# Kernel tuning notes

Hardware: AMD Instinct MI355X
Metric: run time of the kernel (lower is better)

Reference implementation:

```python
import jax, jax.numpy as jnp
import numpy as np

N_HEAD = 16
HEAD_DIM = 64
ROPE_BASE = 10000.0


def _rope_cos_sin(T, dim, dtype):
    inv_freq = 1.0 / (ROPE_BASE ** (np.arange(0, dim, 2, dtype=np.float32) / dim))
    t = np.arange(T, dtype=np.float32)
    freqs = np.outer(t, inv_freq)              # [T, dim/2]
    emb = np.concatenate([freqs, freqs], -1)   # [T, dim]
    return jnp.asarray(np.cos(emb), dtype), jnp.asarray(np.sin(emb), dtype)


def _rotate_half(x):
    x1, x2 = x[..., : x.shape[-1] // 2], x[..., x.shape[-1] // 2 :]
    return jnp.concatenate([-x2, x1], axis=-1)


def setup_inputs() -> dict:
    key = jax.random.key(0)
    k1, k2, k3 = jax.random.split(key, 3)
    B, T, C = 4, 2048, 1024
    x = jax.random.normal(k1, (B, T, C), jnp.float32)
    w_qkv = jax.random.normal(k2, (C, 3 * C), jnp.float32) * (C ** -0.5)
    w_proj = jax.random.normal(k3, (C, C), jnp.float32) * (C ** -0.5)
    return {"x": x, "w_qkv": w_qkv, "w_proj": w_proj}


def reference(x, w_qkv, w_proj):
    B, T, C = x.shape
    H, D = N_HEAD, HEAD_DIM
    qkv = x @ w_qkv                                   # [B, T, 3C]
    q, k, v = jnp.split(qkv, 3, axis=-1)
    # [B, H, T, D]
    q = q.reshape(B, T, H, D).transpose(0, 2, 1, 3)
    k = k.reshape(B, T, H, D).transpose(0, 2, 1, 3)
    v = v.reshape(B, T, H, D).transpose(0, 2, 1, 3)
    cos, sin = _rope_cos_sin(T, D, x.dtype)           # [T, D]
    q = q * cos + _rotate_half(q) * sin
    k = k * cos + _rotate_half(k) * sin
    scale = D ** -0.5
    scores = jnp.einsum("bhqd,bhkd->bhqk", q, k) * scale
    causal = jnp.tril(jnp.ones((T, T), bool))
    scores = jnp.where(causal, scores, jnp.finfo(scores.dtype).min)
    attn = jax.nn.softmax(scores, axis=-1)
    y = jnp.einsum("bhqk,bhkd->bhqd", attn, v)        # [B, H, T, D]
    y = y.transpose(0, 2, 1, 3).reshape(B, T, C)
    return y @ w_proj
```

## Files before the change

kernel.cpp:

```cpp
#include <hip/hip_runtime.h>
#include <cstdint>

typedef unsigned short u16;
typedef __attribute__((ext_vector_type(4))) float f32x4;
typedef __attribute__((ext_vector_type(4))) unsigned short u16x4;
typedef __attribute__((ext_vector_type(8))) unsigned short u16x8;
typedef __attribute__((ext_vector_type(8))) __bf16 bf16x8;

#define DEV __device__ __forceinline__

DEV u16 f2bf(float f) {
  union { float f; uint32_t u; } x{f};
  uint32_t r = (x.u + 0x7fffu + ((x.u >> 16) & 1u)) >> 16;
  return (u16)r;
}

DEV void gl_lds16(const void* g, void* l) {
  __builtin_amdgcn_global_load_lds((__attribute__((address_space(1))) void*)(g),
                                   (__attribute__((address_space(3))) void*)(l),
                                   16, 0, 0);
}

__global__ __launch_bounds__(256) void cast_f2b(const float* __restrict__ in,
                                                u16* __restrict__ out) {
  int i = blockIdx.x * 256 + threadIdx.x;
  float4 v = ((const float4*)in)[i];
  u16x4 o = { f2bf(v.x), f2bf(v.y), f2bf(v.z), f2bf(v.w) };
  ((u16x4*)out)[i] = o;
}

__global__ __launch_bounds__(256) void transpose_cast(const float* __restrict__ in,
                                                      u16* __restrict__ out, int R, int C) {
  __shared__ float tile[64][65];
  const int c0 = blockIdx.x * 64, r0 = blockIdx.y * 64;
  const int tx = threadIdx.x & 63, ty = threadIdx.x >> 6;
  for (int r = ty; r < 64; r += 4) tile[r][tx] = in[(size_t)(r0 + r) * C + c0 + tx];
  __syncthreads();
  for (int r = ty; r < 64; r += 4) out[(size_t)(c0 + r) * R + r0 + tx] = f2bf(tile[tx][r]);
}

template <int EPI>
__global__ __launch_bounds__(256) void gemm_bt(const u16* __restrict__ A,
                                               const u16* __restrict__ Bt,
                                               u16* __restrict__ qo, u16* __restrict__ ko,
                                               u16* __restrict__ vo, float* __restrict__ outf) {
  extern __shared__ char lds_occupancy_pad[];
  const int K = 1024;
  __shared__ __align__(16) u16 As[128 * 64];
  __shared__ __align__(16) u16 Bs[128 * 64];
  const int m0 = blockIdx.y * 128, n0 = blockIdx.x * 128;
  const int tid = threadIdx.x;
  const int w = tid >> 6, lane = tid & 63, quad = lane >> 4, l15 = lane & 15;
  const int mw = (w >> 1) * 64, nw = (w & 1) * 64;

  const int srow = tid >> 3;
  const int schunk = ((tid & 7) ^ (srow & 7)) * 8;

  f32x4 acc[4][4];
#pragma unroll
  for (int i = 0; i < 4; ++i)
#pragma unroll
    for (int j = 0; j < 4; ++j) acc[i][j] = f32x4{0.f, 0.f, 0.f, 0.f};

  const u16* ga0 = A + (size_t)(m0 + srow) * K + schunk;
  const u16* gb0 = Bt + (size_t)(n0 + srow) * K + schunk;

  const int sw7 = l15 & 7;
  int aoff[4], boff[4];
#pragma unroll
  for (int i = 0; i < 4; ++i) aoff[i] = (mw + i * 16 + l15) * 64;
#pragma unroll
  for (int j = 0; j < 4; ++j) boff[j] = (nw + j * 16 + l15) * 64;
  int coff[2];
#pragma unroll
  for (int kk = 0; kk < 2; ++kk) coff[kk] = ((kk * 4 + quad) ^ sw7) * 8;

  for (int k0 = 0; k0 < K; k0 += 64) {
#pragma unroll
    for (int ss = 0; ss < 4; ++ss) {
      gl_lds16(ga0 + (size_t)ss * 32 * K + k0, As + ss * 2048 + tid * 8);
      gl_lds16(gb0 + (size_t)ss * 32 * K + k0, Bs + ss * 2048 + tid * 8);
    }
    __syncthreads();
#pragma unroll
    for (int kk = 0; kk < 2; ++kk) {
      bf16x8 af[4], bfv[4];
#pragma unroll
      for (int i = 0; i < 4; ++i) af[i] = *(const bf16x8*)(As + aoff[i] + coff[kk]);
#pragma unroll
      for (int j = 0; j < 4; ++j) bfv[j] = *(const bf16x8*)(Bs + boff[j] + coff[kk]);
#pragma unroll
      for (int i = 0; i < 4; ++i)
#pragma unroll
        for (int j = 0; j < 4; ++j)
          acc[i][j] = __builtin_amdgcn_mfma_f32_16x16x32_bf16(af[i], bfv[j], acc[i][j], 0, 0, 0);
    }
    __syncthreads();
  }

  if (EPI == 1) {
#pragma unroll
    for (int i = 0; i < 4; ++i)
#pragma unroll
      for (int j = 0; j < 4; ++j)
#pragma unroll
        for (int r = 0; r < 4; ++r) {
          int row = m0 + mw + i * 16 + quad * 4 + r;
          int col = n0 + nw + j * 16 + l15;
          outf[(size_t)row * 1024 + col] = acc[i][j][r];
        }
    return;
  }
  const int s = n0 >> 10;
  const int hh = ((n0 & 1023) + nw) >> 6;
  if (s == 2) {
#pragma unroll
    for (int i = 0; i < 4; ++i)
#pragma unroll
      for (int r = 0; r < 4; ++r) {
        int row = m0 + mw + i * 16 + quad * 4 + r;
        int b = row >> 11, t = row & 2047;
        size_t base = ((size_t)(b * 16 + hh) * 2048 + t) * 64;
#pragma unroll
        for (int j = 0; j < 4; ++j) vo[base + j * 16 + l15] = f2bf(acc[i][j][r]);
      }
  } else {
    u16* dst = (s == 0) ? qo : ko;
    const float QS = (s == 0) ? 0.18033688011112042f : 1.0f;
    const float C1 = -0.4152410118609203f;
    const float R2PI = 0.15915494309189535f;
    const float inv0 = __builtin_amdgcn_exp2f((float)l15 * C1) * R2PI;
    const float inv1 = __builtin_amdgcn_exp2f((float)(16 + l15) * C1) * R2PI;
#pragma unroll
    for (int i = 0; i < 4; ++i)
#pragma unroll
      for (int r = 0; r < 4; ++r) {
        int row = m0 + mw + i * 16 + quad * 4 + r;
        int b = row >> 11, t = row & 2047;
        size_t base = ((size_t)(b * 16 + hh) * 2048 + t) * 64;
        float tf = (float)t;
        float a0 = tf * inv0; a0 -= floorf(a0);
        float a1 = tf * inv1; a1 -= floorf(a1);
        float c0 = __builtin_amdgcn_cosf(a0), s0 = __builtin_amdgcn_sinf(a0);
        float c1 = __builtin_amdgcn_cosf(a1), s1 = __builtin_amdgcn_sinf(a1);
        float x0 = acc[i][0][r], y0 = acc[i][2][r];
        float x1 = acc[i][1][r], y1 = acc[i][3][r];
        dst[base + l15]      = f2bf((x0 * c0 - y0 * s0) * QS);
        dst[base + 32 + l15] = f2bf((y0 * c0 + x0 * s0) * QS);
        dst[base + 16 + l15] = f2bf((x1 * c1 - y1 * s1) * QS);
        dst[base + 48 + l15] = f2bf((y1 * c1 + x1 * s1) * QS);
      }
  }
}

__global__ __launch_bounds__(256) void transpose_v(const u16* __restrict__ v,
                                                   u16* __restrict__ vt) {
  const int bh = blockIdx.y, t0 = blockIdx.x * 64;
  __shared__ __align__(16) u16 tile[64][72];
  const int tid = threadIdx.x;
  const int row = tid >> 3, col = (tid & 7) * 8;
#pragma unroll
  for (int rr = 0; rr < 2; ++rr) {
    int r = row + rr * 32;
    *(u16x8*)(&tile[r][col]) = *(const u16x8*)(v + ((size_t)bh * 2048 + t0 + r) * 64 + col);
  }
  __syncthreads();
#pragma unroll
  for (int rr = 0; rr < 2; ++rr) {
    int d = row + rr * 32;
    u16x8 o;
#pragma unroll
    for (int j = 0; j < 8; ++j) o[j] = tile[col + j][d];
    *(u16x8*)(vt + ((size_t)bh * 64 + d) * 2048 + t0 + col) = o;
  }
}

__global__ __launch_bounds__(256) void attn_kernel(const u16* __restrict__ q,
                                                   const u16* __restrict__ k,
                                                   const u16* __restrict__ vt,
                                                   u16* __restrict__ y) {
  const int T = 2048;
  const int bh = blockIdx.x;
  const int qi = 15 - blockIdx.y;
  const int q0 = qi * 128;
  const int tid = threadIdx.x;
  const int w = tid >> 6, lane = tid & 63, quad = lane >> 4, l15 = lane & 15;
  __shared__ __align__(16) u16 Ks[64 * 64];
  __shared__ __align__(16) u16 Vs[64 * 64];
  __shared__ __align__(16) u16 Pq[4 * 32 * 72];
  u16* Pw = Pq + w * 32 * 72;

  const int sw = l15 & 7;
  int koff[4][2], voff[4][2];
#pragma unroll
  for (int kf = 0; kf < 4; ++kf) {
    koff[kf][0] = (kf * 16 + l15) * 64 + ((quad ^ sw) * 8);
    koff[kf][1] = (kf * 16 + l15) * 64 + (((quad + 4) ^ sw) * 8);
  }
#pragma unroll
  for (int df = 0; df < 4; ++df) {
    voff[df][0] = (df * 16 + l15) * 64 + ((quad ^ sw) * 8);
    voff[df][1] = (df * 16 + l15) * 64 + (((quad + 4) ^ sw) * 8);
  }
  const int pwoff = l15 * 72 + quad * 4;
  const int proff = l15 * 72 + quad * 8;

  const int r_ = tid >> 3, c_ = tid & 7, ssw = r_ & 7;
  const u16* kg = k + (size_t)bh * T * 64;
  const u16* vg = vt + (size_t)bh * 64 * T;
  const int sk0 = r_ * 64 + (c_ ^ ssw) * 8;
  const int sk1 = (r_ + 32) * 64 + (c_ ^ ssw) * 8;
  const int sv0 = r_ * T + (c_ ^ ssw) * 8;
  const int sv1 = (r_ + 32) * T + (c_ ^ ssw) * 8;

  const int b_ = bh >> 4, h_ = bh & 15;
  const int q0w = q0 + w * 32;

  bf16x8 qf_[2][2];
#pragma unroll
  for (int qf = 0; qf < 2; ++qf)
#pragma unroll
    for (int h = 0; h < 2; ++h)
      qf_[qf][h] = *(const bf16x8*)(q + ((size_t)bh * T + q0w + qf * 16 + l15) * 64 + h * 32 + quad * 8);

  f32x4 o[2][4];
  float li[2] = {0.f, 0.f};
#pragma unroll
  for (int qf = 0; qf < 2; ++qf)
#pragma unroll
    for (int df = 0; df < 4; ++df) o[qf][df] = f32x4{0.f, 0.f, 0.f, 0.f};

  const int nit = 2 * qi + 2;

  for (int it = 0; it < nit; ++it) {
    const int kb = it * 64;
    gl_lds16(kg + (size_t)kb * 64 + sk0, Ks + tid * 8);
    gl_lds16(kg + (size_t)kb * 64 + sk1, Ks + 2048 + tid * 8);
    gl_lds16(vg + kb + sv0, Vs + tid * 8);
    gl_lds16(vg + kb + sv1, Vs + 2048 + tid * 8);
    __syncthreads();

    bf16x8 ka[4][2];
#pragma unroll
    for (int kf = 0; kf < 4; ++kf) {
      ka[kf][0] = *(const bf16x8*)(Ks + koff[kf][0]);
      ka[kf][1] = *(const bf16x8*)(Ks + koff[kf][1]);
    }
    f32x4 st[2][4];
#pragma unroll
    for (int kf = 0; kf < 4; ++kf)
#pragma unroll
      for (int qf = 0; qf < 2; ++qf) {
        f32x4 s = f32x4{0.f, 0.f, 0.f, 0.f};
        s = __builtin_amdgcn_mfma_f32_16x16x32_bf16(ka[kf][0], qf_[qf][0], s, 0, 0, 0);
        s = __builtin_amdgcn_mfma_f32_16x16x32_bf16(ka[kf][1], qf_[qf][1], s, 0, 0, 0);
        st[qf][kf] = s;
      }

    if (it >= nit - 2) {
#pragma unroll
      for (int qf = 0; qf < 2; ++qf) {
        const int qrow = q0w + qf * 16 + l15;
#pragma unroll
        for (int kf = 0; kf < 4; ++kf)
#pragma unroll
          for (int r = 0; r < 4; ++r)
            if (kb + kf * 16 + quad * 4 + r > qrow) st[qf][kf][r] = -__builtin_inff();
      }
    }

#pragma unroll
    for (int qf = 0; qf < 2; ++qf) {
      float rs = 0.f;
#pragma unroll
      for (int kf = 0; kf < 4; ++kf) {
        float p0 = __builtin_amdgcn_exp2f(st[qf][kf][0]);
        float p1 = __builtin_amdgcn_exp2f(st[qf][kf][1]);
        float p2 = __builtin_amdgcn_exp2f(st[qf][kf][2]);
        float p3 = __builtin_amdgcn_exp2f(st[qf][kf][3]);
        rs += (p0 + p1) + (p2 + p3);
        union { float f; uint32_t u; } u0{p0}, u1{p1}, u2{p2}, u3{p3};
        uint32_t pk01 = __builtin_amdgcn_perm(u1.u + 0x8000u, u0.u + 0x8000u, 0x07060302u);
        uint32_t pk23 = __builtin_amdgcn_perm(u3.u + 0x8000u, u2.u + 0x8000u, 0x07060302u);
        uint2 pk; pk.x = pk01; pk.y = pk23;
        *(uint2*)(Pw + qf * 16 * 72 + pwoff + kf * 16) = pk;
      }
      li[qf] += rs;
    }

#pragma unroll
    for (int qf = 0; qf < 2; ++qf) {
      bf16x8 pb0 = *(const bf16x8*)(Pw + qf * 16 * 72 + proff);
      bf16x8 pb1 = *(const bf16x8*)(Pw + qf * 16 * 72 + proff + 32);
#pragma unroll
      for (int df = 0; df < 4; ++df) {
        bf16x8 va0 = *(const bf16x8*)(Vs + voff[df][0]);
        bf16x8 va1 = *(const bf16x8*)(Vs + voff[df][1]);
        o[qf][df] = __builtin_amdgcn_mfma_f32_16x16x32_bf16(va0, pb0, o[qf][df], 0, 0, 0);
        o[qf][df] = __builtin_amdgcn_mfma_f32_16x16x32_bf16(va1, pb1, o[qf][df], 0, 0, 0);
      }
    }
    __syncthreads();
  }

#pragma unroll
  for (int qf = 0; qf < 2; ++qf) {
    float l = li[qf];
    l += __shfl_xor(l, 16, 64);
    l += __shfl_xor(l, 32, 64);
    const float inv = 1.f / l;
    const size_t base = ((size_t)b_ * 2048 + q0w + qf * 16 + l15) * 1024 + h_ * 64;
#pragma unroll
    for (int df = 0; df < 4; ++df) {
      u16x4 ov;
#pragma unroll
      for (int r = 0; r < 4; ++r) ov[r] = f2bf(o[qf][df][r] * inv);
      *(u16x4*)(y + base + df * 16 + quad * 4) = ov;
    }
  }
}

extern "C" void kernel_launch(void* const* d_in, const int* in_sizes, int n_in,
                              void* d_out, int out_size, void* d_ws, size_t ws_size,
                              hipStream_t stream) {
  const float* x = (const float*)d_in[0];
  const float* w_qkv = (const float*)d_in[1];
  const float* w_proj = (const float*)d_in[2];
  float* out = (float*)d_out;

  u16* xb = (u16*)d_ws;
  u16* wqkvT = xb + 8388608;
  u16* wprojT = wqkvT + 3145728;
  u16* qb = wprojT + 1048576;
  u16* kbuf = qb + 8388608;
  u16* vb = kbuf + 8388608;
  u16* vtb = vb + 8388608;
  u16* yb = xb;

  cast_f2b<<<8192, 256, 0, stream>>>(x, xb);
  transpose_cast<<<dim3(48, 16), 256, 0, stream>>>(w_qkv, wqkvT, 1024, 3072);
  transpose_cast<<<dim3(16, 16), 256, 0, stream>>>(w_proj, wprojT, 1024, 1024);
  gemm_bt<0><<<dim3(24, 64), 256, 21504, stream>>>(xb, wqkvT, qb, kbuf, vb, nullptr);
  transpose_v<<<dim3(32, 64), 256, 0, stream>>>(vb, vtb);
  attn_kernel<<<dim3(64, 16), 256, 0, stream>>>(qb, kbuf, vtb, yb);
  gemm_bt<1><<<dim3(8, 64), 256, 0, stream>>>(yb, wprojT, nullptr, nullptr, nullptr, out);
}
```

Before: 242.3 us.

## Replace QKV GEMM with 256x256-tile 8-wave double-buffered pipelined kernel

Adds a dedicated QKV projection kernel that uses 256x256 output tiles, 512 threads, and double-buffered direct global-to-LDS loads. The next k-tile's loads are interleaved between MFMA phases, with explicit barriers, setprio and vmcnt waits. A swizzled block index is used for L2 locality. The goal is more operand reuse per LDS byte and overlap of memory with compute compared to the old 128x128 tile GEMM. The cost is heavy register pressure from 32 accumulators per lane, 128 KB of LDS per block, and fragile hand-written wait counts.

```diff
diff --git a/kernel.cpp b/kernel.cpp
--- a/kernel.cpp
+++ b/kernel.cpp
@@ -20,6 +20,8 @@
                                    (__attribute__((address_space(3))) void*)(l),
                                    16, 0, 0);
 }
+
+DEV void bar() { asm volatile("s_barrier" ::: "memory"); }
 
 __global__ __launch_bounds__(256) void cast_f2b(const float* __restrict__ in,
                                                 u16* __restrict__ out) {
@@ -37,6 +39,194 @@
   for (int r = ty; r < 64; r += 4) tile[r][tx] = in[(size_t)(r0 + r) * C + c0 + tx];
   __syncthreads();
   for (int r = ty; r < 64; r += 4) out[(size_t)(c0 + r) * R + r0 + tx] = f2bf(tile[tx][r]);
+}
+
+__global__ __launch_bounds__(512, 2) void gemm256_qkv(const u16* __restrict__ A,
+                                                      const u16* __restrict__ Bt,
+                                                      u16* __restrict__ qo,
+                                                      u16* __restrict__ ko,
+                                                      u16* __restrict__ vo) {
+  __shared__ __align__(16) u16 As[2][2][8192];
+  __shared__ __align__(16) u16 Bs[2][2][8192];
+
+  const int lin = blockIdx.x;
+  const int id = (lin & 7) * 48 + (lin >> 3);
+  const int bx = id % 12, by = id / 12;
+  const int m0 = by * 256, n0 = bx * 256;
+  const int tid = threadIdx.x;
+  const int w = tid >> 6, lane = tid & 63, quad = lane >> 4, l15 = lane & 15;
+  const int wm = w >> 2, wn = w & 3;
+
+  const int rd0 = tid >> 3;
+  const int sch = ((tid & 7) ^ (rd0 & 7)) * 8;
+
+  const u16* gA = A + (size_t)m0 * 1024;
+  const u16* gB = Bt + (size_t)n0 * 1024;
+
+  const int sw = l15 & 7;
+  int coff[2];
+#pragma unroll
+  for (int kk = 0; kk < 2; ++kk) coff[kk] = ((kk * 4 + quad) ^ sw) * 8;
+  const int abase = l15 * 64;
+  const int bbase = ((wn & 1) * 64 + l15) * 64;
+
+  f32x4 acc[8][4];
+#pragma unroll
+  for (int i = 0; i < 8; ++i)
+#pragma unroll
+    for (int j = 0; j < 4; ++j) acc[i][j] = f32x4{0.f, 0.f, 0.f, 0.f};
+
+  auto stage = [&](const u16* panel, u16* lds) {
+    gl_lds16(panel + (size_t)rd0 * 1024 + sch, lds + tid * 8);
+    gl_lds16(panel + (size_t)(rd0 + 64) * 1024 + sch, lds + 4096 + tid * 8);
+  };
+
+  stage(gA, &As[0][0][0]);
+  stage(gA + 131072, &As[0][1][0]);
+  stage(gB, &Bs[0][0][0]);
+  stage(gB + 131072, &Bs[0][1][0]);
+  stage(gA + 64, &As[1][0][0]);
+  stage(gA + 64 + 131072, &As[1][1][0]);
+  stage(gB + 64, &Bs[1][0][0]);
+  stage(gB + 64 + 131072, &Bs[1][1][0]);
+  asm volatile("s_waitcnt vmcnt(8)" ::: "memory");
+  bar();
+
+  auto ktile4 = [&](int b, int sk, bool dostage, bool last) {
+    const u16* Ah = &As[b][wm][0];
+    const u16* Bh = &Bs[b][wn >> 1][0];
+    bf16x8 af[4][2], b0f[2][2], b1f[2][2];
+
+#pragma unroll
+    for (int mf = 0; mf < 4; ++mf)
+#pragma unroll
+      for (int kk = 0; kk < 2; ++kk)
+        af[mf][kk] = *(const bf16x8*)(Ah + abase + mf * 1024 + coff[kk]);
+#pragma unroll
+    for (int nf = 0; nf < 2; ++nf)
+#pragma unroll
+      for (int kk = 0; kk < 2; ++kk)
+        b0f[nf][kk] = *(const bf16x8*)(Bh + bbase + nf * 1024 + coff[kk]);
+    bar();
+    __builtin_amdgcn_s_setprio(1);
+#pragma unroll
+    for (int mf = 0; mf < 4; ++mf)
+#pragma unroll
+      for (int nf = 0; nf < 2; ++nf)
+#pragma unroll
+        for (int kk = 0; kk < 2; ++kk)
+          acc[mf][nf] = __builtin_amdgcn_mfma_f32_16x16x32_bf16(af[mf][kk], b0f[nf][kk],
+                                                                acc[mf][nf], 0, 0, 0);
+    __builtin_amdgcn_s_setprio(0);
+    bar();
+
+#pragma unroll
+    for (int nf = 0; nf < 2; ++nf)
+#pragma unroll
+      for (int kk = 0; kk < 2; ++kk)
+        b1f[nf][kk] = *(const bf16x8*)(Bh + bbase + (2 + nf) * 1024 + coff[kk]);
+    bar();
+    __builtin_amdgcn_s_setprio(1);
+#pragma unroll
+    for (int mf = 0; mf < 4; ++mf)
+#pragma unroll
+      for (int nf = 0; nf < 2; ++nf)
+#pragma unroll
+        for (int kk = 0; kk < 2; ++kk)
+          acc[mf][2 + nf] = __builtin_amdgcn_mfma_f32_16x16x32_bf16(af[mf][kk], b1f[nf][kk],
+                                                                    acc[mf][2 + nf], 0, 0, 0);
+    __builtin_amdgcn_s_setprio(0);
+    bar();
+
+#pragma unroll
+    for (int mf = 0; mf < 4; ++mf)
+#pragma unroll
+      for (int kk = 0; kk < 2; ++kk)
+        af[mf][kk] = *(const bf16x8*)(Ah + abase + (4 + mf) * 1024 + coff[kk]);
+    if (dostage) {
+      stage(gB + sk, &Bs[b][0][0]);
+      stage(gB + sk + 131072, &Bs[b][1][0]);
+    }
+    bar();
+    __builtin_amdgcn_s_setprio(1);
+#pragma unroll
+    for (int mf = 0; mf < 4; ++mf)
+#pragma unroll
+      for (int nf = 0; nf < 2; ++nf)
+#pragma unroll
+        for (int kk = 0; kk < 2; ++kk)
+          acc[4 + mf][2 + nf] = __builtin_amdgcn_mfma_f32_16x16x32_bf16(af[mf][kk], b1f[nf][kk],
+                                                                        acc[4 + mf][2 + nf], 0, 0, 0);
+    __builtin_amdgcn_s_setprio(0);
+    bar();
+
+    if (dostage) {
+      stage(gA + sk, &As[b][0][0]);
+      stage(gA + sk + 131072, &As[b][1][0]);
+    }
+    bar();
+    __builtin_amdgcn_s_setprio(1);
+#pragma unroll
+    for (int mf = 0; mf < 4; ++mf)
+#pragma unroll
+      for (int nf = 0; nf < 2; ++nf)
+#pragma unroll
+        for (int kk = 0; kk < 2; ++kk)
+          acc[4 + mf][nf] = __builtin_amdgcn_mfma_f32_16x16x32_bf16(af[mf][kk], b0f[nf][kk],
+                                                                    acc[4 + mf][nf], 0, 0, 0);
+    __builtin_amdgcn_s_setprio(0);
+    if (last) asm volatile("s_waitcnt vmcnt(0)" ::: "memory");
+    else      asm volatile("s_waitcnt vmcnt(6)" ::: "memory");
+    bar();
+  };
+
+  for (int it = 0; it < 8; ++it) {
+    const bool nl = (it < 7);
+    ktile4(0, it * 128 + 128, nl, !nl);
+    ktile4(1, it * 128 + 192, nl, !nl);
+  }
+
+  const int s = n0 >> 10;
+  const int hh = ((n0 & 1023) >> 6) + wn;
+  const int rowbase = m0 + wm * 128 + quad * 4;
+  if (s == 2) {
+#pragma unroll
+    for (int mf = 0; mf < 8; ++mf)
+#pragma unroll
+      for (int r = 0; r < 4; ++r) {
+        int row = rowbase + mf * 16 + r;
+        int b = row >> 11, t = row & 2047;
+        size_t base = ((size_t)(b * 16 + hh) * 2048 + t) * 64;
+#pragma unroll
+        for (int nf = 0; nf < 4; ++nf) vo[base + nf * 16 + l15] = f2bf(acc[mf][nf][r]);
+      }
+  } else {
+    u16* dst = (s == 0) ? qo : ko;
+    const float QS = (s == 0) ? 0.18033688011112042f : 1.0f;
+    const float C1 = -0.4152410118609203f;
+    const float R2PI = 0.15915494309189535f;
+    const float inv0 = __builtin_amdgcn_exp2f((float)l15 * C1) * R2PI;
+    const float inv1 = __builtin_amdgcn_exp2f((float)(16 + l15) * C1) * R2PI;
+#pragma unroll
+    for (int mf = 0; mf < 8; ++mf)
+#pragma unroll
+      for (int r = 0; r < 4; ++r) {
+        int row = rowbase + mf * 16 + r;
+        int b = row >> 11, t = row & 2047;
+        size_t base = ((size_t)(b * 16 + hh) * 2048 + t) * 64;
+        float tf = (float)t;
+        float a0 = tf * inv0; a0 -= floorf(a0);
+        float a1 = tf * inv1; a1 -= floorf(a1);
+        float c0 = __builtin_amdgcn_cosf(a0), s0 = __builtin_amdgcn_sinf(a0);
+        float c1 = __builtin_amdgcn_cosf(a1), s1 = __builtin_amdgcn_sinf(a1);
+        float x0 = acc[mf][0][r], y0 = acc[mf][2][r];
+        float x1 = acc[mf][1][r], y1 = acc[mf][3][r];
+        dst[base + l15]      = f2bf((x0 * c0 - y0 * s0) * QS);
+        dst[base + 32 + l15] = f2bf((y0 * c0 + x0 * s0) * QS);
+        dst[base + 16 + l15] = f2bf((x1 * c1 - y1 * s1) * QS);
+        dst[base + 48 + l15] = f2bf((y1 * c1 + x1 * s1) * QS);
+      }
+  }
 }
 
 template <int EPI>
@@ -110,46 +300,6 @@
           outf[(size_t)row * 1024 + col] = acc[i][j][r];
         }
     return;
-  }
-  const int s = n0 >> 10;
-  const int hh = ((n0 & 1023) + nw) >> 6;
-  if (s == 2) {
-#pragma unroll
-    for (int i = 0; i < 4; ++i)
-#pragma unroll
-      for (int r = 0; r < 4; ++r) {
-        int row = m0 + mw + i * 16 + quad * 4 + r;
-        int b = row >> 11, t = row & 2047;
-        size_t base = ((size_t)(b * 16 + hh) * 2048 + t) * 64;
-#pragma unroll
-        for (int j = 0; j < 4; ++j) vo[base + j * 16 + l15] = f2bf(acc[i][j][r]);
-      }
-  } else {
-    u16* dst = (s == 0) ? qo : ko;
-    const float QS = (s == 0) ? 0.18033688011112042f : 1.0f;
-    const float C1 = -0.4152410118609203f;
-    const float R2PI = 0.15915494309189535f;
-    const float inv0 = __builtin_amdgcn_exp2f((float)l15 * C1) * R2PI;
-    const float inv1 = __builtin_amdgcn_exp2f((float)(16 + l15) * C1) * R2PI;
-#pragma unroll
-    for (int i = 0; i < 4; ++i)
-#pragma unroll
-      for (int r = 0; r < 4; ++r) {
-        int row = m0 + mw + i * 16 + quad * 4 + r;
-        int b = row >> 11, t = row & 2047;
-        size_t base = ((size_t)(b * 16 + hh) * 2048 + t) * 64;
-        float tf = (float)t;
-        float a0 = tf * inv0; a0 -= floorf(a0);
-        float a1 = tf * inv1; a1 -= floorf(a1);
-        float c0 = __builtin_amdgcn_cosf(a0), s0 = __builtin_amdgcn_sinf(a0);
-        float c1 = __builtin_amdgcn_cosf(a1), s1 = __builtin_amdgcn_sinf(a1);
-        float x0 = acc[i][0][r], y0 = acc[i][2][r];
-        float x1 = acc[i][1][r], y1 = acc[i][3][r];
-        dst[base + l15]      = f2bf((x0 * c0 - y0 * s0) * QS);
-        dst[base + 32 + l15] = f2bf((y0 * c0 + x0 * s0) * QS);
-        dst[base + 16 + l15] = f2bf((x1 * c1 - y1 * s1) * QS);
-        dst[base + 48 + l15] = f2bf((y1 * c1 + x1 * s1) * QS);
-      }
   }
 }
 
@@ -340,7 +490,7 @@
   cast_f2b<<<8192, 256, 0, stream>>>(x, xb);
   transpose_cast<<<dim3(48, 16), 256, 0, stream>>>(w_qkv, wqkvT, 1024, 3072);
   transpose_cast<<<dim3(16, 16), 256, 0, stream>>>(w_proj, wprojT, 1024, 1024);
-  gemm_bt<0><<<dim3(24, 64), 256, 21504, stream>>>(xb, wqkvT, qb, kbuf, vb, nullptr);
+  gemm256_qkv<<<384, 512, 0, stream>>>(xb, wqkvT, qb, kbuf, vb);
   transpose_v<<<dim3(32, 64), 256, 0, stream>>>(vb, vtb);
   attn_kernel<<<dim3(64, 16), 256, 0, stream>>>(qb, kbuf, vtb, yb);
   gemm_bt<1><<<dim3(8, 64), 256, 0, stream>>>(yb, wprojT, nullptr, nullptr, nullptr, out);
```

New measurement: 256.7 us. 1.06x slower.
